# Kernel optimization log

Measured on AMD Instinct MI355X. Metric: run time of the kernel, lower is better.

The kernel has to match this reference:

```python
import jax, jax.numpy as jnp
import numpy as np

N = 1000000   # total nodes
F = 32        # node feature dim
E = 8         # edge feature dim
K = 16        # kernels per degree
COUNTS = [200000, 300000, 300000, 200000]  # focal nodes per degree 1..4
EPS = 1e-8


def _cos_mat(a, b):
    # a: [n, f], b: [k, f] -> cosine sim [n, k]
    num = a @ b.T
    den = jnp.linalg.norm(a, axis=-1)[:, None] * jnp.linalg.norm(b, axis=-1)[None, :]
    return num / jnp.maximum(den, EPS)


def _cos_pairs(a, b):
    # a: [n, d, f], b: [k, d, f] -> mean over d of per-slot cosine sim -> [n, k]
    num = jnp.einsum('ndf,kdf->nkd', a, b)
    den = jnp.linalg.norm(a, axis=-1)[:, None, :] * jnp.linalg.norm(b, axis=-1)[None, :, :]
    return jnp.mean(num / jnp.maximum(den, EPS), axis=-1)


def _deg_score(x, sel, nei, nei_p, nei_e, Wc, Wn, Wp, We, d):
    nd = sel.shape[0]
    x_focal = x[sel]                     # [nd, F] degree-grouped gather
    x_nei = x[nei].reshape(nd, d, F)     # [nd, d, F]
    sc = (_cos_mat(x_focal, Wc) + _cos_pairs(x_nei, Wn)
          + _cos_pairs(nei_p, Wp) + _cos_pairs(nei_e, We)) * 0.25
    return sc                            # [nd, K]


def setup_inputs() -> dict:
    key = jax.random.key(0)
    ks = iter(jax.random.split(key, 64))
    perm = jax.random.permutation(next(ks), N)  # degree buckets partition all nodes
    inp = {"x": jax.random.normal(next(ks), (N, F), jnp.float32)}
    off = 0
    for d in range(1, 5):
        nd = COUNTS[d - 1]
        inp[f"sel{d}"] = perm[off:off + nd]
        off += nd
        inp[f"nei{d}"] = jax.random.randint(next(ks), (nd * d,), 0, N)
        inp[f"nei_p{d}"] = jax.random.normal(next(ks), (nd, d, 3), jnp.float32)
        inp[f"nei_e{d}"] = jax.random.uniform(next(ks), (nd, d, E), jnp.float32)
        inp[f"Wc{d}"] = jax.random.normal(next(ks), (K, F), jnp.float32)
        inp[f"Wn{d}"] = jax.random.normal(next(ks), (K, d, F), jnp.float32)
        inp[f"Wp{d}"] = jax.random.normal(next(ks), (K, d, 3), jnp.float32)
        inp[f"We{d}"] = jax.random.normal(next(ks), (K, d, E), jnp.float32)
    return inp


def reference(x,
              sel1, nei1, nei_p1, nei_e1, Wc1, Wn1, Wp1, We1,
              sel2, nei2, nei_p2, nei_e2, Wc2, Wn2, Wp2, We2,
              sel3, nei3, nei_p3, nei_e3, Wc3, Wn3, Wp3, We3,
              sel4, nei4, nei_p4, nei_e4, Wc4, Wn4, Wp4, We4):
    groups = [
        (sel1, nei1, nei_p1, nei_e1, Wc1, Wn1, Wp1, We1),
        (sel2, nei2, nei_p2, nei_e2, Wc2, Wn2, Wp2, We2),
        (sel3, nei3, nei_p3, nei_e3, Wc3, Wn3, Wp3, We3),
        (sel4, nei4, nei_p4, nei_e4, Wc4, Wn4, Wp4, We4),
    ]
    # equivalent to: fill [sum_K, N] block matrix grouped by degree, reorder
    # columns by argsort of concatenated selected indices, then transpose.
    out = jnp.zeros((N, 4 * K), x.dtype)
    for i, (sel, nei, npos, ne, wc, wn, wp, we) in enumerate(groups):
        sc = _deg_score(x, sel, nei, npos, ne, wc, wn, wp, we, i + 1)
        out = out.at[sel, i * K:(i + 1) * K].set(sc)
    return out
```

## Files before the change

### kernel.cpp

```cpp
#include <hip/hip_runtime.h>
#include <stdint.h>

typedef _Float16 half8 __attribute__((ext_vector_type(8)));
typedef float floatx4 __attribute__((ext_vector_type(4)));
typedef float fvec4 __attribute__((ext_vector_type(4)));

struct WPtrs { const float *wc, *wn, *wp, *we; };

struct PrepArgs {
  const float* x; _Float16* xhat; int N; int nb_norm;
  const float* p[4]; const float* e[4]; _Float16* part[4];
  int nd[4];
  int pb[5];
  WPtrs w[4]; _Float16* psi;
};

template <int D>
__device__ inline void part_one(const PrepArgs& a, int g, int lblk, int tid,
                                float* wl) {
  const float* __restrict__ p  = a.p[g];
  const float* __restrict__ e  = a.e[g];
  _Float16* __restrict__ part  = a.part[g];
  int nd = a.nd[g];

  if (tid < 16 * D) {
    const float* sp = a.w[g].wp + tid * 3;
    float a0 = sp[0], a1 = sp[1], a2 = sp[2];
    float n1 = sqrtf(a0 * a0 + a1 * a1 + a2 * a2);
    float s1 = n1 > 0.f ? 0.25f / (D * n1) : 0.f;
    wl[tid * 11 + 0] = a0 * s1;
    wl[tid * 11 + 1] = a1 * s1;
    wl[tid * 11 + 2] = a2 * s1;
    const float* se = a.w[g].we + tid * 8;
    float b0 = se[0], b1 = se[1], b2 = se[2], b3 = se[3];
    float b4 = se[4], b5 = se[5], b6 = se[6], b7 = se[7];
    float n2 = sqrtf(b0 * b0 + b1 * b1 + b2 * b2 + b3 * b3 +
                     b4 * b4 + b5 * b5 + b6 * b6 + b7 * b7);
    float s2 = n2 > 0.f ? 0.25f / (D * n2) : 0.f;
    wl[tid * 11 + 3]  = b0 * s2; wl[tid * 11 + 4]  = b1 * s2;
    wl[tid * 11 + 5]  = b2 * s2; wl[tid * 11 + 6]  = b3 * s2;
    wl[tid * 11 + 7]  = b4 * s2; wl[tid * 11 + 8]  = b5 * s2;
    wl[tid * 11 + 9]  = b6 * s2; wl[tid * 11 + 10] = b7 * s2;
  }
  __syncthreads();

  int node = lblk * 256 + tid;
  if (node >= nd) return;

  float ph[D][3], eh[D][8];
#pragma unroll
  for (int s = 0; s < D; ++s) {
    const float* pp = p + ((size_t)node * D + s) * 3;
    float a0 = pp[0], a1 = pp[1], a2 = pp[2];
    float n1 = sqrtf(a0 * a0 + a1 * a1 + a2 * a2);
    float r1 = n1 > 0.f ? 1.f / n1 : 0.f;
    ph[s][0] = a0 * r1; ph[s][1] = a1 * r1; ph[s][2] = a2 * r1;

    const fvec4* ee = reinterpret_cast<const fvec4*>(e + ((size_t)node * D + s) * 8);
    fvec4 e0 = ee[0], e1 = ee[1];
    float n2 = sqrtf(e0[0] * e0[0] + e0[1] * e0[1] + e0[2] * e0[2] + e0[3] * e0[3] +
                     e1[0] * e1[0] + e1[1] * e1[1] + e1[2] * e1[2] + e1[3] * e1[3]);
    float r2 = n2 > 0.f ? 1.f / n2 : 0.f;
    eh[s][0] = e0[0] * r2; eh[s][1] = e0[1] * r2;
    eh[s][2] = e0[2] * r2; eh[s][3] = e0[3] * r2;
    eh[s][4] = e1[0] * r2; eh[s][5] = e1[1] * r2;
    eh[s][6] = e1[2] * r2; eh[s][7] = e1[3] * r2;
  }

  half8 h0, h1;
#pragma unroll
  for (int k = 0; k < 16; ++k) {
    float t = 0.f;
#pragma unroll
    for (int s = 0; s < D; ++s) {
      const float* w = wl + (k * D + s) * 11;
      t += ph[s][0] * w[0] + ph[s][1] * w[1] + ph[s][2] * w[2];
#pragma unroll
      for (int j = 0; j < 8; ++j) t += eh[s][j] * w[3 + j];
    }
    if (k < 8) h0[k] = (_Float16)t; else h1[k - 8] = (_Float16)t;
  }
  _Float16* dst = part + (size_t)node * 16;
  *reinterpret_cast<half8*>(dst)     = h0;
  *reinterpret_cast<half8*>(dst + 8) = h1;
}

__global__ __launch_bounds__(256) void k_prep(PrepArgs a) {
  __shared__ float wl[16 * 4 * 11];
  int bid = blockIdx.x, tid = threadIdx.x;

  if (bid < a.nb_norm) {
    int row = bid * 64 + (tid >> 2);
    int q   = tid & 3;
    if (row >= a.N) return;
    const fvec4* xr = reinterpret_cast<const fvec4*>(a.x + (size_t)row * 32 + q * 8);
    fvec4 va = xr[0];
    fvec4 vb = xr[1];
    float ss = va[0] * va[0] + va[1] * va[1] + va[2] * va[2] + va[3] * va[3] +
               vb[0] * vb[0] + vb[1] * vb[1] + vb[2] * vb[2] + vb[3] * vb[3];
    ss += __shfl_xor(ss, 1);
    ss += __shfl_xor(ss, 2);
    float rn = ss > 0.f ? rsqrtf(ss) : 0.f;
    half8 h;
    h[0] = (_Float16)(va[0] * rn); h[1] = (_Float16)(va[1] * rn);
    h[2] = (_Float16)(va[2] * rn); h[3] = (_Float16)(va[3] * rn);
    h[4] = (_Float16)(vb[0] * rn); h[5] = (_Float16)(vb[1] * rn);
    h[6] = (_Float16)(vb[2] * rn); h[7] = (_Float16)(vb[3] * rn);
    *reinterpret_cast<half8*>(a.xhat + (size_t)row * 32 + q * 8) = h;
    return;
  }

  int b2 = bid - a.nb_norm;
  if (b2 < a.pb[4]) {
    if      (b2 < a.pb[1]) part_one<1>(a, 0, b2,           tid, wl);
    else if (b2 < a.pb[2]) part_one<2>(a, 1, b2 - a.pb[1], tid, wl);
    else if (b2 < a.pb[3]) part_one<3>(a, 2, b2 - a.pb[2], tid, wl);
    else                   part_one<4>(a, 3, b2 - a.pb[3], tid, wl);
    return;
  }

  int g = b2 - a.pb[4];
  int d = g + 1;
  int KD = 32 * (1 + d);
  _Float16* pg = a.psi + (size_t)g * (16 * 160);

  int k     = tid & 15;
  int piece = tid >> 4;
  if (piece > d) return;
  const float* src;
  float scale;
  if (piece == 0) { src = a.w[g].wc + k * 32;                          scale = 0.25f; }
  else            { src = a.w[g].wn + (size_t)(k * d + piece - 1) * 32; scale = 0.25f / d; }
  float ss = 0.f;
  for (int j = 0; j < 32; ++j) ss += src[j] * src[j];
  float n  = sqrtf(ss);
  float sc = n > 0.f ? scale / n : 0.f;
  _Float16* dst = pg + k * KD + 32 * piece;
  for (int j = 0; j < 32; ++j) dst[j] = (_Float16)(src[j] * sc);
}

struct MainArgs {
  const _Float16* xhat;
  const _Float16* part[4];
  const _Float16* psi;
  const int* sel[4];
  const int* nei[4];
  float* out;
  int nd[4];
  int blkOff[5];
};

template <int D, int NCH>
__device__ inline void main_one(const MainArgs& a, int g, int blk) {
  constexpr int NF = 1 + D;
  constexpr int KD = 32 * NF;

  const _Float16* xhat = a.xhat;
  const _Float16* part = a.part[g];
  const _Float16* psi  = a.psi + (size_t)g * (16 * 160);
  const int* sel = a.sel[g];
  const int* nei = a.nei[g];
  int nd = a.nd[g];

  int wave    = threadIdx.x >> 6;
  int lane    = threadIdx.x & 63;
  int nchunks = (nd + 15) >> 4;
  int chunk0  = (blk * 4 + wave) * NCH;
  if (chunk0 >= nchunks) return;
  int r = lane & 15;
  int c = lane >> 4;

  half8 bx[NF];
  {
    const _Float16* pb = psi + (size_t)r * KD + c * 8;
#pragma unroll
    for (int t = 0; t < NF; ++t)
      bx[t] = *reinterpret_cast<const half8*>(pb + 32 * t);
  }

  int riA[NCH];
  int sidx[NCH];
  int gidx[NCH][D];
#pragma unroll
  for (int u = 0; u < NCH; ++u) {
    int chunk = chunk0 + u;
    int ri = (chunk < nchunks) ? (chunk * 16 + r) : 0;
    if (ri > nd - 1) ri = nd - 1;
    riA[u]  = ri;
    sidx[u] = sel[ri];
  }
#pragma unroll
  for (int u = 0; u < NCH; ++u)
#pragma unroll
    for (int s = 0; s < D; ++s)
      gidx[u][s] = nei[(size_t)riA[u] * D + s];

  floatx4 acc[NCH];
#pragma unroll
  for (int u = 0; u < NCH; ++u) {
    int i0 = (chunk0 + u) << 4;
#pragma unroll
    for (int j = 0; j < 4; ++j) {
      int n = i0 + c * 4 + j;
      if (n > nd - 1) n = nd - 1;
      acc[u][j] = (float)part[(size_t)n * 16 + r];
    }
  }

  half8 af[NCH][NF];
#pragma unroll
  for (int u = 0; u < NCH; ++u) {
    af[u][0] = *reinterpret_cast<const half8*>(xhat + (size_t)sidx[u] * 32 + c * 8);
#pragma unroll
    for (int s = 0; s < D; ++s)
      af[u][1 + s] = *reinterpret_cast<const half8*>(xhat + (size_t)gidx[u][s] * 32 + c * 8);
  }

#pragma unroll
  for (int u = 0; u < NCH; ++u)
#pragma unroll
    for (int t = 0; t < NF; ++t)
      acc[u] = __builtin_amdgcn_mfma_f32_16x16x32_f16(af[u][t], bx[t], acc[u], 0, 0, 0);

#pragma unroll
  for (int u = 0; u < NCH; ++u) {
    int chunk = chunk0 + u;
    if (chunk >= nchunks) break;
    int i0 = chunk << 4;
#pragma unroll
    for (int j = 0; j < 4; ++j) {
      int n  = i0 + c * 4 + j;
      int so = __shfl(sidx[u], c * 4 + j);
      if (n < nd) {
        float* orow = a.out + (size_t)so * 64 + r;
#pragma unroll
        for (int q = 0; q < 4; ++q)
          orow[q * 16] = (q == D - 1) ? acc[u][j] : 0.f;
      }
    }
  }
}

__global__ __launch_bounds__(256) void k_main(MainArgs a) {
  int bid = blockIdx.x;
  if (bid < a.blkOff[1])      main_one<1, 6>(a, 0, bid);
  else if (bid < a.blkOff[2]) main_one<2, 5>(a, 1, bid - a.blkOff[1]);
  else if (bid < a.blkOff[3]) main_one<3, 4>(a, 2, bid - a.blkOff[2]);
  else                        main_one<4, 3>(a, 3, bid - a.blkOff[3]);
}

extern "C" void kernel_launch(void* const* d_in, const int* in_sizes, int n_in,
                              void* d_out, int out_size, void* d_ws, size_t ws_size,
                              hipStream_t stream) {
  const float* x = (const float*)d_in[0];
  int N = in_sizes[0] / 32;

  PrepArgs pa;
  MainArgs ma;
  pa.x = x; pa.N = N;
  int nd[4];
  for (int g = 0; g < 4; ++g) {
    int b = 1 + g * 8;
    ma.sel[g]  = (const int*)d_in[b + 0];
    ma.nei[g]  = (const int*)d_in[b + 1];
    pa.p[g]    = (const float*)d_in[b + 2];
    pa.e[g]    = (const float*)d_in[b + 3];
    pa.w[g].wc = (const float*)d_in[b + 4];
    pa.w[g].wn = (const float*)d_in[b + 5];
    pa.w[g].wp = (const float*)d_in[b + 6];
    pa.w[g].we = (const float*)d_in[b + 7];
    nd[g] = in_sizes[b];
    pa.nd[g] = nd[g];
    ma.nd[g] = nd[g];
  }
  ma.out = (float*)d_out;

  char* ws = (char*)d_ws;
  auto align256 = [](size_t o) { return (o + 255) & ~(size_t)255; };
  _Float16* xhat = (_Float16*)ws;
  size_t off = (size_t)N * 32 * 2;
  for (int g = 0; g < 4; ++g) {
    off = align256(off);
    pa.part[g] = (_Float16*)(ws + off);
    ma.part[g] = pa.part[g];
    off += (size_t)nd[g] * 16 * 2;
  }
  off = align256(off);
  _Float16* psi = (_Float16*)(ws + off);
  pa.psi = psi;
  ma.psi = psi;
  pa.xhat = xhat;
  ma.xhat = xhat;

  pa.nb_norm = (N + 63) / 64;
  pa.pb[0] = 0;
  for (int g = 0; g < 4; ++g) pa.pb[g + 1] = pa.pb[g] + (nd[g] + 255) / 256;
  int prep_blocks = pa.nb_norm + pa.pb[4] + 4;

  const int NCHg[4] = {6, 5, 4, 3};
  ma.blkOff[0] = 0;
  for (int g = 0; g < 4; ++g) {
    int ch = (nd[g] + 15) / 16;
    int perBlk = 4 * NCHg[g];
    ma.blkOff[g + 1] = ma.blkOff[g] + (ch + perBlk - 1) / perBlk;
  }

  k_prep<<<prep_blocks, 256, 0, stream>>>(pa);
  k_main<<<ma.blkOff[4], 256, 0, stream>>>(ma);
}
```

Before: 196.4 us.

## Compute edge/position partial scores with MFMA and split norm into separate kernel

The per-node position/edge cosine partial scores are now computed with 16x16x32 f16 MFMA instructions. Normalized inputs and scaled weights are staged in LDS as padded half rows, replacing the scalar FP32 dot-product loops. The x-row normalization moves out of the combined prep kernel into its own launch, adding one kernel launch. The change trades scalar ALU work for LDS staging, extra zero padding, scattered 2-byte output stores and fp16 rounding of the inputs.

```diff
diff --git a/kernel.cpp b/kernel.cpp
--- a/kernel.cpp
+++ b/kernel.cpp
@@ -7,8 +7,27 @@
 
 struct WPtrs { const float *wc, *wn, *wp, *we; };
 
-struct PrepArgs {
-  const float* x; _Float16* xhat; int N; int nb_norm;
+__global__ __launch_bounds__(256) void k_norm(const float* __restrict__ x,
+                                              _Float16* __restrict__ xhat, int N) {
+  int t = blockIdx.x * 256 + threadIdx.x;
+  int row = t >> 2, q = t & 3;
+  if (row >= N) return;
+  const fvec4* xr = reinterpret_cast<const fvec4*>(x + (size_t)row * 32 + q * 8);
+  fvec4 va = xr[0], vb = xr[1];
+  float ss = va[0] * va[0] + va[1] * va[1] + va[2] * va[2] + va[3] * va[3] +
+             vb[0] * vb[0] + vb[1] * vb[1] + vb[2] * vb[2] + vb[3] * vb[3];
+  ss += __shfl_xor(ss, 1);
+  ss += __shfl_xor(ss, 2);
+  float rn = ss > 0.f ? rsqrtf(ss) : 0.f;
+  half8 h;
+  h[0] = (_Float16)(va[0] * rn); h[1] = (_Float16)(va[1] * rn);
+  h[2] = (_Float16)(va[2] * rn); h[3] = (_Float16)(va[3] * rn);
+  h[4] = (_Float16)(vb[0] * rn); h[5] = (_Float16)(vb[1] * rn);
+  h[6] = (_Float16)(vb[2] * rn); h[7] = (_Float16)(vb[3] * rn);
+  *reinterpret_cast<half8*>(xhat + (size_t)row * 32 + q * 8) = h;
+}
+
+struct PartArgs {
   const float* p[4]; const float* e[4]; _Float16* part[4];
   int nd[4];
   int pb[5];
@@ -16,110 +35,127 @@
 };
 
 template <int D>
-__device__ inline void part_one(const PrepArgs& a, int g, int lblk, int tid,
-                                float* wl) {
-  const float* __restrict__ p  = a.p[g];
-  const float* __restrict__ e  = a.e[g];
-  _Float16* __restrict__ part  = a.part[g];
+__device__ inline void part_mfma(const PartArgs& a, int g, int lblk, int tid,
+                                 _Float16* lds) {
+  constexpr int K16 = 16 * D;
+  constexpr int K32 = ((D + 1) / 2) * 32;
+  constexpr int NM  = K32 / 32;
+  constexpr int RS  = K32 + 8;
+
+  const float* __restrict__ p = a.p[g];
+  const float* __restrict__ e = a.e[g];
+  _Float16* __restrict__ part = a.part[g];
   int nd = a.nd[g];
 
+  _Float16* aLds = lds;
+  _Float16* bLds = lds + 256 * RS;
+
   if (tid < 16 * D) {
-    const float* sp = a.w[g].wp + tid * 3;
+    int k = tid / D, s = tid % D;
+    const float* sp = a.w[g].wp + (size_t)tid * 3;
     float a0 = sp[0], a1 = sp[1], a2 = sp[2];
     float n1 = sqrtf(a0 * a0 + a1 * a1 + a2 * a2);
     float s1 = n1 > 0.f ? 0.25f / (D * n1) : 0.f;
-    wl[tid * 11 + 0] = a0 * s1;
-    wl[tid * 11 + 1] = a1 * s1;
-    wl[tid * 11 + 2] = a2 * s1;
-    const float* se = a.w[g].we + tid * 8;
+    const float* se = a.w[g].we + (size_t)tid * 8;
     float b0 = se[0], b1 = se[1], b2 = se[2], b3 = se[3];
     float b4 = se[4], b5 = se[5], b6 = se[6], b7 = se[7];
     float n2 = sqrtf(b0 * b0 + b1 * b1 + b2 * b2 + b3 * b3 +
                      b4 * b4 + b5 * b5 + b6 * b6 + b7 * b7);
     float s2 = n2 > 0.f ? 0.25f / (D * n2) : 0.f;
-    wl[tid * 11 + 3]  = b0 * s2; wl[tid * 11 + 4]  = b1 * s2;
-    wl[tid * 11 + 5]  = b2 * s2; wl[tid * 11 + 6]  = b3 * s2;
-    wl[tid * 11 + 7]  = b4 * s2; wl[tid * 11 + 8]  = b5 * s2;
-    wl[tid * 11 + 9]  = b6 * s2; wl[tid * 11 + 10] = b7 * s2;
-  }
-  __syncthreads();
+    half8 h0, h1;
+    h0[0] = (_Float16)(a0 * s1); h0[1] = (_Float16)(a1 * s1);
+    h0[2] = (_Float16)(a2 * s1); h0[3] = (_Float16)0.f;
+    h0[4] = (_Float16)(b0 * s2); h0[5] = (_Float16)(b1 * s2);
+    h0[6] = (_Float16)(b2 * s2); h0[7] = (_Float16)(b3 * s2);
+    h1[0] = (_Float16)(b4 * s2); h1[1] = (_Float16)(b5 * s2);
+    h1[2] = (_Float16)(b6 * s2); h1[3] = (_Float16)(b7 * s2);
+    h1[4] = (_Float16)0.f; h1[5] = (_Float16)0.f;
+    h1[6] = (_Float16)0.f; h1[7] = (_Float16)0.f;
+    _Float16* w = bLds + k * RS + s * 16;
+    *reinterpret_cast<half8*>(w)     = h0;
+    *reinterpret_cast<half8*>(w + 8) = h1;
+  }
+  if (K32 > K16 && tid < 16) {
+    half8 z = {};
+    _Float16* w = bLds + tid * RS + K16;
+    *reinterpret_cast<half8*>(w)     = z;
+    *reinterpret_cast<half8*>(w + 8) = z;
+  }
 
   int node = lblk * 256 + tid;
-  if (node >= nd) return;
-
-  float ph[D][3], eh[D][8];
+  int nc = node < nd ? node : nd - 1;
+  _Float16* arow = aLds + tid * RS;
 #pragma unroll
   for (int s = 0; s < D; ++s) {
-    const float* pp = p + ((size_t)node * D + s) * 3;
+    const float* pp = p + ((size_t)nc * D + s) * 3;
     float a0 = pp[0], a1 = pp[1], a2 = pp[2];
     float n1 = sqrtf(a0 * a0 + a1 * a1 + a2 * a2);
     float r1 = n1 > 0.f ? 1.f / n1 : 0.f;
-    ph[s][0] = a0 * r1; ph[s][1] = a1 * r1; ph[s][2] = a2 * r1;
-
-    const fvec4* ee = reinterpret_cast<const fvec4*>(e + ((size_t)node * D + s) * 8);
+    const fvec4* ee = reinterpret_cast<const fvec4*>(e + ((size_t)nc * D + s) * 8);
     fvec4 e0 = ee[0], e1 = ee[1];
     float n2 = sqrtf(e0[0] * e0[0] + e0[1] * e0[1] + e0[2] * e0[2] + e0[3] * e0[3] +
                      e1[0] * e1[0] + e1[1] * e1[1] + e1[2] * e1[2] + e1[3] * e1[3]);
     float r2 = n2 > 0.f ? 1.f / n2 : 0.f;
-    eh[s][0] = e0[0] * r2; eh[s][1] = e0[1] * r2;
-    eh[s][2] = e0[2] * r2; eh[s][3] = e0[3] * r2;
-    eh[s][4] = e1[0] * r2; eh[s][5] = e1[1] * r2;
-    eh[s][6] = e1[2] * r2; eh[s][7] = e1[3] * r2;
-  }
-
-  half8 h0, h1;
-#pragma unroll
-  for (int k = 0; k < 16; ++k) {
-    float t = 0.f;
-#pragma unroll
-    for (int s = 0; s < D; ++s) {
-      const float* w = wl + (k * D + s) * 11;
-      t += ph[s][0] * w[0] + ph[s][1] * w[1] + ph[s][2] * w[2];
-#pragma unroll
-      for (int j = 0; j < 8; ++j) t += eh[s][j] * w[3 + j];
+    half8 h0, h1;
+    h0[0] = (_Float16)(a0 * r1); h0[1] = (_Float16)(a1 * r1);
+    h0[2] = (_Float16)(a2 * r1); h0[3] = (_Float16)0.f;
+    h0[4] = (_Float16)(e0[0] * r2); h0[5] = (_Float16)(e0[1] * r2);
+    h0[6] = (_Float16)(e0[2] * r2); h0[7] = (_Float16)(e0[3] * r2);
+    h1[0] = (_Float16)(e1[0] * r2); h1[1] = (_Float16)(e1[1] * r2);
+    h1[2] = (_Float16)(e1[2] * r2); h1[3] = (_Float16)(e1[3] * r2);
+    h1[4] = (_Float16)0.f; h1[5] = (_Float16)0.f;
+    h1[6] = (_Float16)0.f; h1[7] = (_Float16)0.f;
+    *reinterpret_cast<half8*>(arow + s * 16)     = h0;
+    *reinterpret_cast<half8*>(arow + s * 16 + 8) = h1;
+  }
+  if (K32 > K16) {
+    half8 z = {};
+    *reinterpret_cast<half8*>(arow + K16)     = z;
+    *reinterpret_cast<half8*>(arow + K16 + 8) = z;
+  }
+
+  __syncthreads();
+
+  int lane = tid & 63, wv = tid >> 6;
+  int r = lane & 15, c = lane >> 4;
+
+  half8 bf[NM];
+#pragma unroll
+  for (int m = 0; m < NM; ++m)
+    bf[m] = *reinterpret_cast<const half8*>(bLds + r * RS + m * 32 + c * 8);
+
+#pragma unroll
+  for (int q = 0; q < 4; ++q) {
+    half8 af[NM];
+#pragma unroll
+    for (int m = 0; m < NM; ++m)
+      af[m] = *reinterpret_cast<const half8*>(aLds + (wv * 64 + q * 16 + r) * RS + m * 32 + c * 8);
+    floatx4 acc = {0.f, 0.f, 0.f, 0.f};
+#pragma unroll
+    for (int m = 0; m < NM; ++m)
+      acc = __builtin_amdgcn_mfma_f32_16x16x32_f16(af[m], bf[m], acc, 0, 0, 0);
+    int nb = lblk * 256 + wv * 64 + q * 16;
+#pragma unroll
+    for (int j = 0; j < 4; ++j) {
+      int ng = nb + c * 4 + j;
+      if (ng < nd) part[(size_t)ng * 16 + r] = (_Float16)acc[j];
     }
-    if (k < 8) h0[k] = (_Float16)t; else h1[k - 8] = (_Float16)t;
-  }
-  _Float16* dst = part + (size_t)node * 16;
-  *reinterpret_cast<half8*>(dst)     = h0;
-  *reinterpret_cast<half8*>(dst + 8) = h1;
-}
-
-__global__ __launch_bounds__(256) void k_prep(PrepArgs a) {
-  __shared__ float wl[16 * 4 * 11];
+  }
+}
+
+__global__ __launch_bounds__(256) void k_part(PartArgs a) {
+  __shared__ _Float16 lds[256 * 72 + 16 * 72];
   int bid = blockIdx.x, tid = threadIdx.x;
 
-  if (bid < a.nb_norm) {
-    int row = bid * 64 + (tid >> 2);
-    int q   = tid & 3;
-    if (row >= a.N) return;
-    const fvec4* xr = reinterpret_cast<const fvec4*>(a.x + (size_t)row * 32 + q * 8);
-    fvec4 va = xr[0];
-    fvec4 vb = xr[1];
-    float ss = va[0] * va[0] + va[1] * va[1] + va[2] * va[2] + va[3] * va[3] +
-               vb[0] * vb[0] + vb[1] * vb[1] + vb[2] * vb[2] + vb[3] * vb[3];
-    ss += __shfl_xor(ss, 1);
-    ss += __shfl_xor(ss, 2);
-    float rn = ss > 0.f ? rsqrtf(ss) : 0.f;
-    half8 h;
-    h[0] = (_Float16)(va[0] * rn); h[1] = (_Float16)(va[1] * rn);
-    h[2] = (_Float16)(va[2] * rn); h[3] = (_Float16)(va[3] * rn);
-    h[4] = (_Float16)(vb[0] * rn); h[5] = (_Float16)(vb[1] * rn);
-    h[6] = (_Float16)(vb[2] * rn); h[7] = (_Float16)(vb[3] * rn);
-    *reinterpret_cast<half8*>(a.xhat + (size_t)row * 32 + q * 8) = h;
+  if (bid < a.pb[4]) {
+    if      (bid < a.pb[1]) part_mfma<1>(a, 0, bid,           tid, lds);
+    else if (bid < a.pb[2]) part_mfma<2>(a, 1, bid - a.pb[1], tid, lds);
+    else if (bid < a.pb[3]) part_mfma<3>(a, 2, bid - a.pb[2], tid, lds);
+    else                    part_mfma<4>(a, 3, bid - a.pb[3], tid, lds);
     return;
   }
 
-  int b2 = bid - a.nb_norm;
-  if (b2 < a.pb[4]) {
-    if      (b2 < a.pb[1]) part_one<1>(a, 0, b2,           tid, wl);
-    else if (b2 < a.pb[2]) part_one<2>(a, 1, b2 - a.pb[1], tid, wl);
-    else if (b2 < a.pb[3]) part_one<3>(a, 2, b2 - a.pb[2], tid, wl);
-    else                   part_one<4>(a, 3, b2 - a.pb[3], tid, wl);
-    return;
-  }
-
-  int g = b2 - a.pb[4];
+  int g = bid - a.pb[4];
   int d = g + 1;
   int KD = 32 * (1 + d);
   _Float16* pg = a.psi + (size_t)g * (16 * 160);
@@ -129,7 +165,7 @@
   if (piece > d) return;
   const float* src;
   float scale;
-  if (piece == 0) { src = a.w[g].wc + k * 32;                          scale = 0.25f; }
+  if (piece == 0) { src = a.w[g].wc + k * 32;                           scale = 0.25f; }
   else            { src = a.w[g].wn + (size_t)(k * d + piece - 1) * 32; scale = 0.25f / d; }
   float ss = 0.f;
   for (int j = 0; j < 32; ++j) ss += src[j] * src[j];
@@ -255,23 +291,22 @@
   const float* x = (const float*)d_in[0];
   int N = in_sizes[0] / 32;
 
-  PrepArgs pa;
+  PartArgs pra;
   MainArgs ma;
-  pa.x = x; pa.N = N;
   int nd[4];
   for (int g = 0; g < 4; ++g) {
     int b = 1 + g * 8;
-    ma.sel[g]  = (const int*)d_in[b + 0];
-    ma.nei[g]  = (const int*)d_in[b + 1];
-    pa.p[g]    = (const float*)d_in[b + 2];
-    pa.e[g]    = (const float*)d_in[b + 3];
-    pa.w[g].wc = (const float*)d_in[b + 4];
-    pa.w[g].wn = (const float*)d_in[b + 5];
-    pa.w[g].wp = (const float*)d_in[b + 6];
-    pa.w[g].we = (const float*)d_in[b + 7];
+    ma.sel[g]   = (const int*)d_in[b + 0];
+    ma.nei[g]   = (const int*)d_in[b + 1];
+    pra.p[g]    = (const float*)d_in[b + 2];
+    pra.e[g]    = (const float*)d_in[b + 3];
+    pra.w[g].wc = (const float*)d_in[b + 4];
+    pra.w[g].wn = (const float*)d_in[b + 5];
+    pra.w[g].wp = (const float*)d_in[b + 6];
+    pra.w[g].we = (const float*)d_in[b + 7];
     nd[g] = in_sizes[b];
-    pa.nd[g] = nd[g];
-    ma.nd[g] = nd[g];
+    pra.nd[g] = nd[g];
+    ma.nd[g]  = nd[g];
   }
   ma.out = (float*)d_out;
 
@@ -281,21 +316,18 @@
   size_t off = (size_t)N * 32 * 2;
   for (int g = 0; g < 4; ++g) {
     off = align256(off);
-    pa.part[g] = (_Float16*)(ws + off);
-    ma.part[g] = pa.part[g];
+    pra.part[g] = (_Float16*)(ws + off);
+    ma.part[g]  = pra.part[g];
     off += (size_t)nd[g] * 16 * 2;
   }
   off = align256(off);
   _Float16* psi = (_Float16*)(ws + off);
-  pa.psi = psi;
-  ma.psi = psi;
-  pa.xhat = xhat;
+  pra.psi = psi;
+  ma.psi  = psi;
   ma.xhat = xhat;
 
-  pa.nb_norm = (N + 63) / 64;
-  pa.pb[0] = 0;
-  for (int g = 0; g < 4; ++g) pa.pb[g + 1] = pa.pb[g] + (nd[g] + 255) / 256;
-  int prep_blocks = pa.nb_norm + pa.pb[4] + 4;
+  pra.pb[0] = 0;
+  for (int g = 0; g < 4; ++g) pra.pb[g + 1] = pra.pb[g] + (nd[g] + 255) / 256;
 
   const int NCHg[4] = {6, 5, 4, 3};
   ma.blkOff[0] = 0;
@@ -305,6 +337,7 @@
     ma.blkOff[g + 1] = ma.blkOff[g] + (ch + perBlk - 1) / perBlk;
   }
 
-  k_prep<<<prep_blocks, 256, 0, stream>>>(pa);
+  k_norm<<<(N * 4 + 255) / 256, 256, 0, stream>>>(x, xhat, N);
+  k_part<<<pra.pb[4] + 4, 256, 0, stream>>>(pra);
   k_main<<<ma.blkOff[4], 256, 0, stream>>>(ma);
 }
```

Measured after the change: 194.2 us. Within noise of the previous version (-1.1%).

## Compute position/edge partial scores with MFMA instead of scalar FMAs

Applied to the files above, without the earlier changes.

The per-node position and edge cosine partial scores are now computed as a small fp16 matrix product on the matrix cores. Each thread writes its normalized slot features into an LDS row, and each lane builds its share of the weight operand in registers. Each wave then issues 16x16x32 MFMAs over its 64 nodes. This replaces the per-thread scalar dot-product loops over 16 kernels and removes the block-wide barrier used for the shared weight table. The cost is a much larger LDS allocation (36 KB) for every k_prep block, including the norm blocks, which may reduce occupancy. The scattered 2-byte output stores may also write less efficiently than the old 16-byte vector stores.

```diff
diff --git a/kernel.cpp b/kernel.cpp
--- a/kernel.cpp
+++ b/kernel.cpp
@@ -16,77 +16,110 @@
 };
 
 template <int D>
-__device__ inline void part_one(const PrepArgs& a, int g, int lblk, int tid,
-                                float* wl) {
-  const float* __restrict__ p  = a.p[g];
-  const float* __restrict__ e  = a.e[g];
-  _Float16* __restrict__ part  = a.part[g];
+__device__ inline void part_mfma(const PrepArgs& a, int g, int lblk, int tid,
+                                 _Float16* lds) {
+  constexpr int K16 = 16 * D;
+  constexpr int K32 = ((D + 1) / 2) * 32;
+  constexpr int NM  = K32 / 32;
+  constexpr int RS  = K32 + 8;
+
+  const float* __restrict__ p = a.p[g];
+  const float* __restrict__ e = a.e[g];
+  _Float16* __restrict__ part = a.part[g];
   int nd = a.nd[g];
 
-  if (tid < 16 * D) {
-    const float* sp = a.w[g].wp + tid * 3;
-    float a0 = sp[0], a1 = sp[1], a2 = sp[2];
-    float n1 = sqrtf(a0 * a0 + a1 * a1 + a2 * a2);
-    float s1 = n1 > 0.f ? 0.25f / (D * n1) : 0.f;
-    wl[tid * 11 + 0] = a0 * s1;
-    wl[tid * 11 + 1] = a1 * s1;
-    wl[tid * 11 + 2] = a2 * s1;
-    const float* se = a.w[g].we + tid * 8;
-    float b0 = se[0], b1 = se[1], b2 = se[2], b3 = se[3];
-    float b4 = se[4], b5 = se[5], b6 = se[6], b7 = se[7];
-    float n2 = sqrtf(b0 * b0 + b1 * b1 + b2 * b2 + b3 * b3 +
-                     b4 * b4 + b5 * b5 + b6 * b6 + b7 * b7);
-    float s2 = n2 > 0.f ? 0.25f / (D * n2) : 0.f;
-    wl[tid * 11 + 3]  = b0 * s2; wl[tid * 11 + 4]  = b1 * s2;
-    wl[tid * 11 + 5]  = b2 * s2; wl[tid * 11 + 6]  = b3 * s2;
-    wl[tid * 11 + 7]  = b4 * s2; wl[tid * 11 + 8]  = b5 * s2;
-    wl[tid * 11 + 9]  = b6 * s2; wl[tid * 11 + 10] = b7 * s2;
-  }
-  __syncthreads();
+  int lane = tid & 63, wv = tid >> 6;
+  int r = lane & 15, c = lane >> 4;
 
   int node = lblk * 256 + tid;
-  if (node >= nd) return;
-
-  float ph[D][3], eh[D][8];
+  int nc = node < nd ? node : nd - 1;
+  _Float16* arow = lds + (size_t)tid * RS;
 #pragma unroll
   for (int s = 0; s < D; ++s) {
-    const float* pp = p + ((size_t)node * D + s) * 3;
+    const float* pp = p + ((size_t)nc * D + s) * 3;
     float a0 = pp[0], a1 = pp[1], a2 = pp[2];
     float n1 = sqrtf(a0 * a0 + a1 * a1 + a2 * a2);
     float r1 = n1 > 0.f ? 1.f / n1 : 0.f;
-    ph[s][0] = a0 * r1; ph[s][1] = a1 * r1; ph[s][2] = a2 * r1;
-
-    const fvec4* ee = reinterpret_cast<const fvec4*>(e + ((size_t)node * D + s) * 8);
+    const fvec4* ee = reinterpret_cast<const fvec4*>(e + ((size_t)nc * D + s) * 8);
     fvec4 e0 = ee[0], e1 = ee[1];
     float n2 = sqrtf(e0[0] * e0[0] + e0[1] * e0[1] + e0[2] * e0[2] + e0[3] * e0[3] +
                      e1[0] * e1[0] + e1[1] * e1[1] + e1[2] * e1[2] + e1[3] * e1[3]);
     float r2 = n2 > 0.f ? 1.f / n2 : 0.f;
-    eh[s][0] = e0[0] * r2; eh[s][1] = e0[1] * r2;
-    eh[s][2] = e0[2] * r2; eh[s][3] = e0[3] * r2;
-    eh[s][4] = e1[0] * r2; eh[s][5] = e1[1] * r2;
-    eh[s][6] = e1[2] * r2; eh[s][7] = e1[3] * r2;
-  }
-
-  half8 h0, h1;
-#pragma unroll
-  for (int k = 0; k < 16; ++k) {
-    float t = 0.f;
-#pragma unroll
-    for (int s = 0; s < D; ++s) {
-      const float* w = wl + (k * D + s) * 11;
-      t += ph[s][0] * w[0] + ph[s][1] * w[1] + ph[s][2] * w[2];
-#pragma unroll
-      for (int j = 0; j < 8; ++j) t += eh[s][j] * w[3 + j];
+    half8 h0, h1;
+    h0[0] = (_Float16)(a0 * r1); h0[1] = (_Float16)(a1 * r1);
+    h0[2] = (_Float16)(a2 * r1); h0[3] = (_Float16)0.f;
+    h0[4] = (_Float16)(e0[0] * r2); h0[5] = (_Float16)(e0[1] * r2);
+    h0[6] = (_Float16)(e0[2] * r2); h0[7] = (_Float16)(e0[3] * r2);
+    h1[0] = (_Float16)(e1[0] * r2); h1[1] = (_Float16)(e1[1] * r2);
+    h1[2] = (_Float16)(e1[2] * r2); h1[3] = (_Float16)(e1[3] * r2);
+    h1[4] = (_Float16)0.f; h1[5] = (_Float16)0.f;
+    h1[6] = (_Float16)0.f; h1[7] = (_Float16)0.f;
+    *reinterpret_cast<half8*>(arow + s * 16)     = h0;
+    *reinterpret_cast<half8*>(arow + s * 16 + 8) = h1;
+  }
+  if (K32 > K16) {
+    half8 z = {};
+    *reinterpret_cast<half8*>(arow + K16)     = z;
+    *reinterpret_cast<half8*>(arow + K16 + 8) = z;
+  }
+
+  half8 bf[NM];
+#pragma unroll
+  for (int m = 0; m < NM; ++m) {
+    int s = 2 * m + (c >> 1);
+    if (s < D) {
+      const float* sp = a.w[g].wp + ((size_t)r * D + s) * 3;
+      float a0 = sp[0], a1 = sp[1], a2 = sp[2];
+      float n1 = sqrtf(a0 * a0 + a1 * a1 + a2 * a2);
+      float s1 = n1 > 0.f ? 0.25f / (D * n1) : 0.f;
+      const float* se = a.w[g].we + ((size_t)r * D + s) * 8;
+      float b0 = se[0], b1 = se[1], b2 = se[2], b3 = se[3];
+      float b4 = se[4], b5 = se[5], b6 = se[6], b7 = se[7];
+      float n2 = sqrtf(b0 * b0 + b1 * b1 + b2 * b2 + b3 * b3 +
+                       b4 * b4 + b5 * b5 + b6 * b6 + b7 * b7);
+      float s2 = n2 > 0.f ? 0.25f / (D * n2) : 0.f;
+      half8 h;
+      if ((c & 1) == 0) {
+        h[0] = (_Float16)(a0 * s1); h[1] = (_Float16)(a1 * s1);
+        h[2] = (_Float16)(a2 * s1); h[3] = (_Float16)0.f;
+        h[4] = (_Float16)(b0 * s2); h[5] = (_Float16)(b1 * s2);
+        h[6] = (_Float16)(b2 * s2); h[7] = (_Float16)(b3 * s2);
+      } else {
+        h[0] = (_Float16)(b4 * s2); h[1] = (_Float16)(b5 * s2);
+        h[2] = (_Float16)(b6 * s2); h[3] = (_Float16)(b7 * s2);
+        h[4] = (_Float16)0.f; h[5] = (_Float16)0.f;
+        h[6] = (_Float16)0.f; h[7] = (_Float16)0.f;
+      }
+      bf[m] = h;
+    } else {
+      bf[m] = half8{};
     }
-    if (k < 8) h0[k] = (_Float16)t; else h1[k - 8] = (_Float16)t;
-  }
-  _Float16* dst = part + (size_t)node * 16;
-  *reinterpret_cast<half8*>(dst)     = h0;
-  *reinterpret_cast<half8*>(dst + 8) = h1;
+  }
+
+  __builtin_amdgcn_wave_barrier();
+
+#pragma unroll
+  for (int q = 0; q < 4; ++q) {
+    half8 af[NM];
+#pragma unroll
+    for (int m = 0; m < NM; ++m)
+      af[m] = *reinterpret_cast<const half8*>(
+          lds + (size_t)(wv * 64 + q * 16 + r) * RS + m * 32 + c * 8);
+    floatx4 acc = {0.f, 0.f, 0.f, 0.f};
+#pragma unroll
+    for (int m = 0; m < NM; ++m)
+      acc = __builtin_amdgcn_mfma_f32_16x16x32_f16(af[m], bf[m], acc, 0, 0, 0);
+    int nb = lblk * 256 + wv * 64 + q * 16;
+#pragma unroll
+    for (int j = 0; j < 4; ++j) {
+      int ng = nb + c * 4 + j;
+      if (ng < nd) part[(size_t)ng * 16 + r] = (_Float16)acc[j];
+    }
+  }
 }
 
 __global__ __launch_bounds__(256) void k_prep(PrepArgs a) {
-  __shared__ float wl[16 * 4 * 11];
+  __shared__ _Float16 lds[256 * 72];
   int bid = blockIdx.x, tid = threadIdx.x;
 
   if (bid < a.nb_norm) {
@@ -94,8 +127,7 @@
     int q   = tid & 3;
     if (row >= a.N) return;
     const fvec4* xr = reinterpret_cast<const fvec4*>(a.x + (size_t)row * 32 + q * 8);
-    fvec4 va = xr[0];
-    fvec4 vb = xr[1];
+    fvec4 va = xr[0], vb = xr[1];
     float ss = va[0] * va[0] + va[1] * va[1] + va[2] * va[2] + va[3] * va[3] +
                vb[0] * vb[0] + vb[1] * vb[1] + vb[2] * vb[2] + vb[3] * vb[3];
     ss += __shfl_xor(ss, 1);
@@ -112,10 +144,10 @@
 
   int b2 = bid - a.nb_norm;
   if (b2 < a.pb[4]) {
-    if      (b2 < a.pb[1]) part_one<1>(a, 0, b2,           tid, wl);
-    else if (b2 < a.pb[2]) part_one<2>(a, 1, b2 - a.pb[1], tid, wl);
-    else if (b2 < a.pb[3]) part_one<3>(a, 2, b2 - a.pb[2], tid, wl);
-    else                   part_one<4>(a, 3, b2 - a.pb[3], tid, wl);
+    if      (b2 < a.pb[1]) part_mfma<1>(a, 0, b2,           tid, lds);
+    else if (b2 < a.pb[2]) part_mfma<2>(a, 1, b2 - a.pb[1], tid, lds);
+    else if (b2 < a.pb[3]) part_mfma<3>(a, 2, b2 - a.pb[2], tid, lds);
+    else                   part_mfma<4>(a, 3, b2 - a.pb[3], tid, lds);
     return;
   }
 
@@ -129,7 +161,7 @@
   if (piece > d) return;
   const float* src;
   float scale;
-  if (piece == 0) { src = a.w[g].wc + k * 32;                          scale = 0.25f; }
+  if (piece == 0) { src = a.w[g].wc + k * 32;                           scale = 0.25f; }
   else            { src = a.w[g].wn + (size_t)(k * d + piece - 1) * 32; scale = 0.25f / d; }
   float ss = 0.f;
   for (int j = 0; j < 32; ++j) ss += src[j] * src[j];
@@ -289,8 +321,8 @@
   _Float16* psi = (_Float16*)(ws + off);
   pa.psi = psi;
   ma.psi = psi;
+  ma.xhat = xhat;
   pa.xhat = xhat;
-  ma.xhat = xhat;
 
   pa.nb_norm = (N + 63) / 64;
   pa.pb[0] = 0;
```

After: 191.3 us. 1.03x faster.
